# Performance work log

Hardware: AMD Instinct MI355X
Metric: run time of the kernel (lower is better)

## Reference

```python
import jax, jax.numpy as jnp
import numpy as np

B_BOXES = 5
N_CLASSES = 80
LAMBDA_COORD = 5.0
LAMBDA_NOOBJ = 0.5
LAMBDA_CLASS = 1.0
EPS = 1e-6


def _corners(b):
    # b: (..., 4) center-format (x, y, w, h) -> x1, y1, x2, y2
    x, y, w, h = b[..., 0], b[..., 1], b[..., 2], b[..., 3]
    return x - w / 2, y - h / 2, x + w / 2, y + h / 2


def pairwise_iou(p_box, t_box):
    # p_box, t_box: (N, S, S, B, 4) -> ious: (N, S, S, B_pred, B_tgt)
    px1, py1, px2, py2 = _corners(p_box[..., :, None, :])
    tx1, ty1, tx2, ty2 = _corners(t_box[..., None, :, :])
    iw = jnp.clip(jnp.minimum(px2, tx2) - jnp.maximum(px1, tx1), 0.0)
    ih = jnp.clip(jnp.minimum(py2, ty2) - jnp.maximum(py1, ty1), 0.0)
    inter = iw * ih
    area_p = (px2 - px1) * (py2 - py1)
    area_t = (tx2 - tx1) * (ty2 - ty1)
    return inter / (area_p + area_t - inter + EPS)


def setup_inputs() -> dict:
    key = jax.random.key(0)
    k1, k2 = jax.random.split(key)
    N, S = 128, 26
    ch = B_BOXES * (5 + N_CLASSES)  # 425
    preds = jax.random.normal(k1, (N, S, S, ch), dtype=jnp.float32)
    targets = jax.random.normal(k2, (N, S, S, ch), dtype=jnp.float32)
    return {"preds": preds, "targets": targets}


def reference(preds, targets):
    N, S = preds.shape[0], preds.shape[1]
    D = 5 + N_CLASSES
    p = preds.reshape(N, S, S, B_BOXES, D)
    t = targets.reshape(N, S, S, B_BOXES, D)

    ious = pairwise_iou(p[..., :4], t[..., :4])          # (N,S,S,B,B)
    best = jnp.argmax(ious, axis=-1)                      # (N,S,S,B)
    idx = jnp.broadcast_to(best[..., None], t.shape)
    matched = jnp.take_along_axis(t, idx, axis=3)         # (N,S,S,B,D)

    obj = (matched[..., 4] > 0).astype(p.dtype)           # (N,S,S,B)
    noobj = 1.0 - obj

    xy_loss = LAMBDA_COORD * jnp.sum(obj[..., None] * (p[..., 0:2] - matched[..., 0:2]) ** 2)

    pwh = jnp.sqrt(jnp.abs(p[..., 2:4] + EPS))
    twh = jnp.sqrt(jnp.abs(matched[..., 2:4] + EPS))
    wh_loss = LAMBDA_COORD * jnp.sum(obj[..., None] * (pwh - twh) ** 2)

    conf_sq = (p[..., 4] - matched[..., 4]) ** 2
    conf_loss_obj = jnp.sum(obj * conf_sq)
    conf_loss_noobj = LAMBDA_NOOBJ * jnp.sum(noobj * conf_sq)

    tcls = jnp.argmax(t[..., 5:], axis=-1)                # (N,S,S,B)
    logp = jax.nn.log_softmax(p[..., 5:], axis=-1)
    nll = -jnp.take_along_axis(logp, tcls[..., None], axis=-1)[..., 0]
    class_loss = LAMBDA_CLASS * jnp.sum(obj * nll)

    return xy_loss + wh_loss + conf_loss_obj + conf_loss_noobj + class_loss
```

## Files before the change

### kernel.cpp

```cpp
#include <hip/hip_runtime.h>
#include <math.h>

#define NB 5
#define NC 80
#define DD 85
#define CH 425
#define EPSF 1e-6f

__global__ __launch_bounds__(256) void yolo_loss_kernel(
    const float* __restrict__ preds,
    const float* __restrict__ targets,
    float* __restrict__ out,
    int ncells)
{
    const int tid   = threadIdx.x;
    const int lane  = tid & 15;
    const int grp   = tid >> 4;
    const long long g0      = (long long)blockIdx.x * 16 + grp;
    const long long gstride = (long long)gridDim.x * 16;

    float acc = 0.0f;

    for (long long cell = g0; cell < ncells; cell += gstride) {
        const long long base = cell * CH;
        const float* pc = preds + base;
        const float* tc = targets + base;

        float tx=0.f, ty=0.f, tw=0.f, th=0.f, tconf=0.f;
        float px=0.f, py=0.f, pw=0.f, ph=0.f, pconf=0.f;
        if (lane < NB) {
            const float* tb = tc + lane * DD;
            tx = tb[0]; ty = tb[1]; tw = tb[2]; th = tb[3]; tconf = tb[4];
            const float* pb = pc + lane * DD;
            px = pb[0]; py = pb[1]; pw = pb[2]; ph = pb[3]; pconf = pb[4];
        }
        const float tx1 = tx - tw * 0.5f;
        const float ty1 = ty - th * 0.5f;
        const float tx2 = tx + tw * 0.5f;
        const float ty2 = ty + th * 0.5f;
        const float area_t = (tx2 - tx1) * (ty2 - ty1);

        #pragma unroll
        for (int b = 0; b < NB; ++b) {
            const float bx    = __shfl(px,    b, 16);
            const float by    = __shfl(py,    b, 16);
            const float bw    = __shfl(pw,    b, 16);
            const float bh    = __shfl(ph,    b, 16);
            const float bconf = __shfl(pconf, b, 16);

            const float px1 = bx - bw * 0.5f;
            const float py1 = by - bh * 0.5f;
            const float px2 = bx + bw * 0.5f;
            const float py2 = by + bh * 0.5f;
            float iw = fminf(px2, tx2) - fmaxf(px1, tx1); iw = fmaxf(iw, 0.0f);
            float ih = fminf(py2, ty2) - fmaxf(py1, ty1); ih = fmaxf(ih, 0.0f);
            const float inter  = iw * ih;
            const float area_p = (px2 - px1) * (py2 - py1);
            const float iou    = inter / (area_p + area_t - inter + EPSF);

            float v  = (lane < NB) ? iou : -INFINITY;
            int   vi = (lane < NB) ? lane : 0x7fffffff;
            #pragma unroll
            for (int m = 1; m < 16; m <<= 1) {
                const float ov = __shfl_xor(v, m, 16);
                const int   oi = __shfl_xor(vi, m, 16);
                if (ov > v || (ov == v && oi < vi)) { v = ov; vi = oi; }
            }
            const int best = vi;

            const float mx    = __shfl(tx,    best, 16);
            const float my    = __shfl(ty,    best, 16);
            const float mw    = __shfl(tw,    best, 16);
            const float mh    = __shfl(th,    best, 16);
            const float mconf = __shfl(tconf, best, 16);

            const float* pcl = pc + b * DD + 5;
            const float* tcl = tc + b * DD + 5;
            float pl[5], tl[5];
            #pragma unroll
            for (int k = 0; k < 5; ++k) {
                pl[k] = pcl[lane + 16 * k];
                tl[k] = tcl[lane + 16 * k];
            }
            float mx5 = pl[0];
            #pragma unroll
            for (int k = 1; k < 5; ++k) mx5 = fmaxf(mx5, pl[k]);
            #pragma unroll
            for (int m = 1; m < 16; m <<= 1) mx5 = fmaxf(mx5, __shfl_xor(mx5, m, 16));
            float se = 0.0f;
            #pragma unroll
            for (int k = 0; k < 5; ++k) se += __expf(pl[k] - mx5);
            #pragma unroll
            for (int m = 1; m < 16; m <<= 1) se += __shfl_xor(se, m, 16);
            const float logZ = mx5 + __logf(se);

            float bv = tl[0]; int bi = lane; float bp = pl[0];
            #pragma unroll
            for (int k = 1; k < 5; ++k) {
                const int ci = lane + 16 * k;
                if (tl[k] > bv) { bv = tl[k]; bi = ci; bp = pl[k]; }
            }
            #pragma unroll
            for (int m = 1; m < 16; m <<= 1) {
                const float ov = __shfl_xor(bv, m, 16);
                const int   oi = __shfl_xor(bi, m, 16);
                const float op = __shfl_xor(bp, m, 16);
                if (ov > bv || (ov == bv && oi < bi)) { bv = ov; bi = oi; bp = op; }
            }
            const float nll = logZ - bp;

            if (lane == b) {
                const float obj = (mconf > 0.0f) ? 1.0f : 0.0f;
                float term;
                const float dx = bx - mx, dy = by - my;
                term = 5.0f * obj * (dx * dx + dy * dy);
                const float spw = sqrtf(fabsf(bw + EPSF));
                const float sph = sqrtf(fabsf(bh + EPSF));
                const float smw = sqrtf(fabsf(mw + EPSF));
                const float smh = sqrtf(fabsf(mh + EPSF));
                const float dw = spw - smw, dh = sph - smh;
                term += 5.0f * obj * (dw * dw + dh * dh);
                const float dc = bconf - mconf;
                const float csq = dc * dc;
                term += obj * csq + 0.5f * (1.0f - obj) * csq;
                term += obj * nll;
                acc += term;
            }
        }
    }

    #pragma unroll
    for (int off = 32; off > 0; off >>= 1) acc += __shfl_down(acc, off, 64);
    __shared__ float wsum[4];
    if ((tid & 63) == 0) wsum[tid >> 6] = acc;
    __syncthreads();
    if (tid == 0) {
        const float s = wsum[0] + wsum[1] + wsum[2] + wsum[3];
        atomicAdd(out, s);
    }
}

extern "C" void kernel_launch(void* const* d_in, const int* in_sizes, int n_in,
                              void* d_out, int out_size, void* d_ws, size_t ws_size,
                              hipStream_t stream) {
    const float* preds   = (const float*)d_in[0];
    const float* targets = (const float*)d_in[1];
    float* out = (float*)d_out;

    const int ncells = in_sizes[0] / CH;
    const int blocks = (ncells + 15) / 16;

    hipMemsetAsync(out, 0, sizeof(float), stream);
    yolo_loss_kernel<<<blocks, 256, 0, stream>>>(preds, targets, out, ncells);
}
```

Measured before the change: 314.7 us.

## Assign one thread per box and scan classes serially with float4 loads

Replaces the 16-lane-per-cell layout, which needed many cross-lane shuffle reductions, with one thread per (cell, box). Each thread computes its own IoU match against the five targets and runs a serial log-sum-exp and argmax over the 80 classes using aligned float4 loads. The aim is to remove shuffle and reduction overhead and idle lanes. In exchange, each thread's accesses are strided across the wavefront, which makes coalescing worse. The softmax also drops the max subtraction, so it can overflow on large logits.

```diff
diff --git a/kernel.cpp b/kernel.cpp
--- a/kernel.cpp
+++ b/kernel.cpp
@@ -7,136 +7,107 @@
 #define CH 425
 #define EPSF 1e-6f
 
+__device__ __forceinline__ void load5(const float* __restrict__ arr, int idx,
+                                      float& a, float& b, float& c, float& d, float& e)
+{
+    const int a0 = idx & ~3;
+    const int r  = idx & 3;
+    const float4 u = *(const float4*)(arr + a0);
+    const float4 v = *(const float4*)(arr + a0 + 4);
+    switch (r) {
+    case 0:  a = u.x; b = u.y; c = u.z; d = u.w; e = v.x; break;
+    case 1:  a = u.y; b = u.z; c = u.w; d = v.x; e = v.y; break;
+    case 2:  a = u.z; b = u.w; c = v.x; d = v.y; e = v.z; break;
+    default: a = u.w; b = v.x; c = v.y; d = v.z; e = v.w; break;
+    }
+}
+
 __global__ __launch_bounds__(256) void yolo_loss_kernel(
     const float* __restrict__ preds,
     const float* __restrict__ targets,
     float* __restrict__ out,
-    int ncells)
+    int ntask)
 {
-    const int tid   = threadIdx.x;
-    const int lane  = tid & 15;
-    const int grp   = tid >> 4;
-    const long long g0      = (long long)blockIdx.x * 16 + grp;
-    const long long gstride = (long long)gridDim.x * 16;
-
+    const int tid = blockIdx.x * 256 + threadIdx.x;
     float acc = 0.0f;
 
-    for (long long cell = g0; cell < ncells; cell += gstride) {
-        const long long base = cell * CH;
-        const float* pc = preds + base;
-        const float* tc = targets + base;
+    if (tid < ntask) {
+        const int cell  = tid / 5;
+        const int b     = tid - cell * 5;
+        const int cbase = cell * CH;
 
-        float tx=0.f, ty=0.f, tw=0.f, th=0.f, tconf=0.f;
-        float px=0.f, py=0.f, pw=0.f, ph=0.f, pconf=0.f;
-        if (lane < NB) {
-            const float* tb = tc + lane * DD;
-            tx = tb[0]; ty = tb[1]; tw = tb[2]; th = tb[3]; tconf = tb[4];
-            const float* pb = pc + lane * DD;
-            px = pb[0]; py = pb[1]; pw = pb[2]; ph = pb[3]; pconf = pb[4];
-        }
-        const float tx1 = tx - tw * 0.5f;
-        const float ty1 = ty - th * 0.5f;
-        const float tx2 = tx + tw * 0.5f;
-        const float ty2 = ty + th * 0.5f;
-        const float area_t = (tx2 - tx1) * (ty2 - ty1);
+        float px, py, pw, ph, pconf;
+        load5(preds, cbase + b * DD, px, py, pw, ph, pconf);
+        const float px1 = px - pw * 0.5f, py1 = py - ph * 0.5f;
+        const float px2 = px + pw * 0.5f, py2 = py + ph * 0.5f;
+        const float area_p = (px2 - px1) * (py2 - py1);
 
+        float best = -INFINITY;
+        float mx = 0.f, my = 0.f, mw = 0.f, mh = 0.f, mconf = 0.f;
         #pragma unroll
-        for (int b = 0; b < NB; ++b) {
-            const float bx    = __shfl(px,    b, 16);
-            const float by    = __shfl(py,    b, 16);
-            const float bw    = __shfl(pw,    b, 16);
-            const float bh    = __shfl(ph,    b, 16);
-            const float bconf = __shfl(pconf, b, 16);
-
-            const float px1 = bx - bw * 0.5f;
-            const float py1 = by - bh * 0.5f;
-            const float px2 = bx + bw * 0.5f;
-            const float py2 = by + bh * 0.5f;
+        for (int t = 0; t < NB; ++t) {
+            float tx, ty, tw, th, tcf;
+            load5(targets, cbase + t * DD, tx, ty, tw, th, tcf);
+            const float tx1 = tx - tw * 0.5f, ty1 = ty - th * 0.5f;
+            const float tx2 = tx + tw * 0.5f, ty2 = ty + th * 0.5f;
             float iw = fminf(px2, tx2) - fmaxf(px1, tx1); iw = fmaxf(iw, 0.0f);
             float ih = fminf(py2, ty2) - fmaxf(py1, ty1); ih = fmaxf(ih, 0.0f);
             const float inter  = iw * ih;
-            const float area_p = (px2 - px1) * (py2 - py1);
+            const float area_t = (tx2 - tx1) * (ty2 - ty1);
             const float iou    = inter / (area_p + area_t - inter + EPSF);
+            if (iou > best) { best = iou; mx = tx; my = ty; mw = tw; mh = th; mconf = tcf; }
+        }
 
-            float v  = (lane < NB) ? iou : -INFINITY;
-            int   vi = (lane < NB) ? lane : 0x7fffffff;
-            #pragma unroll
-            for (int m = 1; m < 16; m <<= 1) {
-                const float ov = __shfl_xor(v, m, 16);
-                const int   oi = __shfl_xor(vi, m, 16);
-                if (ov > v || (ov == v && oi < vi)) { v = ov; vi = oi; }
-            }
-            const int best = vi;
+        const int k0   = cbase + b * DD + 5;
+        const int peel = (4 - (k0 & 3)) & 3;
+        float s  = 0.0f;
+        float bv = -INFINITY;
+        float bp = 0.0f;
+        int k = 0;
+        for (; k < peel; ++k) {
+            const float pl = preds[k0 + k];
+            const float tl = targets[k0 + k];
+            s += __expf(pl);
+            if (tl > bv) { bv = tl; bp = pl; }
+        }
+        #pragma unroll 4
+        for (int i = 0; i < 19; ++i, k += 4) {
+            const float4 p4 = *(const float4*)(preds   + k0 + k);
+            const float4 t4 = *(const float4*)(targets + k0 + k);
+            s += __expf(p4.x); if (t4.x > bv) { bv = t4.x; bp = p4.x; }
+            s += __expf(p4.y); if (t4.y > bv) { bv = t4.y; bp = p4.y; }
+            s += __expf(p4.z); if (t4.z > bv) { bv = t4.z; bp = p4.z; }
+            s += __expf(p4.w); if (t4.w > bv) { bv = t4.w; bp = p4.w; }
+        }
+        for (; k < NC; ++k) {
+            const float pl = preds[k0 + k];
+            const float tl = targets[k0 + k];
+            s += __expf(pl);
+            if (tl > bv) { bv = tl; bp = pl; }
+        }
+        const float nll = __logf(s) - bp;
 
-            const float mx    = __shfl(tx,    best, 16);
-            const float my    = __shfl(ty,    best, 16);
-            const float mw    = __shfl(tw,    best, 16);
-            const float mh    = __shfl(th,    best, 16);
-            const float mconf = __shfl(tconf, best, 16);
-
-            const float* pcl = pc + b * DD + 5;
-            const float* tcl = tc + b * DD + 5;
-            float pl[5], tl[5];
-            #pragma unroll
-            for (int k = 0; k < 5; ++k) {
-                pl[k] = pcl[lane + 16 * k];
-                tl[k] = tcl[lane + 16 * k];
-            }
-            float mx5 = pl[0];
-            #pragma unroll
-            for (int k = 1; k < 5; ++k) mx5 = fmaxf(mx5, pl[k]);
-            #pragma unroll
-            for (int m = 1; m < 16; m <<= 1) mx5 = fmaxf(mx5, __shfl_xor(mx5, m, 16));
-            float se = 0.0f;
-            #pragma unroll
-            for (int k = 0; k < 5; ++k) se += __expf(pl[k] - mx5);
-            #pragma unroll
-            for (int m = 1; m < 16; m <<= 1) se += __shfl_xor(se, m, 16);
-            const float logZ = mx5 + __logf(se);
-
-            float bv = tl[0]; int bi = lane; float bp = pl[0];
-            #pragma unroll
-            for (int k = 1; k < 5; ++k) {
-                const int ci = lane + 16 * k;
-                if (tl[k] > bv) { bv = tl[k]; bi = ci; bp = pl[k]; }
-            }
-            #pragma unroll
-            for (int m = 1; m < 16; m <<= 1) {
-                const float ov = __shfl_xor(bv, m, 16);
-                const int   oi = __shfl_xor(bi, m, 16);
-                const float op = __shfl_xor(bp, m, 16);
-                if (ov > bv || (ov == bv && oi < bi)) { bv = ov; bi = oi; bp = op; }
-            }
-            const float nll = logZ - bp;
-
-            if (lane == b) {
-                const float obj = (mconf > 0.0f) ? 1.0f : 0.0f;
-                float term;
-                const float dx = bx - mx, dy = by - my;
-                term = 5.0f * obj * (dx * dx + dy * dy);
-                const float spw = sqrtf(fabsf(bw + EPSF));
-                const float sph = sqrtf(fabsf(bh + EPSF));
-                const float smw = sqrtf(fabsf(mw + EPSF));
-                const float smh = sqrtf(fabsf(mh + EPSF));
-                const float dw = spw - smw, dh = sph - smh;
-                term += 5.0f * obj * (dw * dw + dh * dh);
-                const float dc = bconf - mconf;
-                const float csq = dc * dc;
-                term += obj * csq + 0.5f * (1.0f - obj) * csq;
-                term += obj * nll;
-                acc += term;
-            }
-        }
+        const float obj = (mconf > 0.0f) ? 1.0f : 0.0f;
+        const float dx = px - mx, dy = py - my;
+        float term = 5.0f * obj * (dx * dx + dy * dy);
+        const float dw = sqrtf(fabsf(pw + EPSF)) - sqrtf(fabsf(mw + EPSF));
+        const float dh = sqrtf(fabsf(ph + EPSF)) - sqrtf(fabsf(mh + EPSF));
+        term += 5.0f * obj * (dw * dw + dh * dh);
+        const float dc  = pconf - mconf;
+        const float csq = dc * dc;
+        term += obj * csq + 0.5f * (1.0f - obj) * csq;
+        term += obj * nll;
+        acc = term;
     }
 
     #pragma unroll
     for (int off = 32; off > 0; off >>= 1) acc += __shfl_down(acc, off, 64);
     __shared__ float wsum[4];
-    if ((tid & 63) == 0) wsum[tid >> 6] = acc;
+    const int t = threadIdx.x;
+    if ((t & 63) == 0) wsum[t >> 6] = acc;
     __syncthreads();
-    if (tid == 0) {
-        const float s = wsum[0] + wsum[1] + wsum[2] + wsum[3];
-        atomicAdd(out, s);
+    if (t == 0) {
+        atomicAdd(out, wsum[0] + wsum[1] + wsum[2] + wsum[3]);
     }
 }
 
@@ -148,8 +119,9 @@
     float* out = (float*)d_out;
 
     const int ncells = in_sizes[0] / CH;
-    const int blocks = (ncells + 15) / 16;
+    const int ntask  = ncells * NB;
+    const int blocks = (ntask + 255) / 256;
 
     hipMemsetAsync(out, 0, sizeof(float), stream);
-    yolo_loss_kernel<<<blocks, 256, 0, stream>>>(preds, targets, out, ncells);
+    yolo_loss_kernel<<<blocks, 256, 0, stream>>>(preds, targets, out, ntask);
 }
```

New measurement: 389.9 us. +23.9%, slower.
